# Kernel optimization log

Measured on AMD Instinct MI355X. Metric: run time of the kernel, lower is better.

## Reference

```python
import jax, jax.numpy as jnp
import numpy as np

B, S, HID, NH = 8, 1024, 1024, 16
HD = HID // NH


def setup_inputs() -> dict:
    key = jax.random.key(0)
    ks = jax.random.split(key, 7)
    scale = 1.0 / np.sqrt(HID)
    return {
        "x": jax.random.normal(ks[0], (B, S, HID), dtype=jnp.float32),
        "attention_mask": jax.random.uniform(ks[1], (B, 1, S, S), dtype=jnp.float32),
        "Wq": jax.random.normal(ks[2], (HID, HID), dtype=jnp.float32) * scale,
        "bq": jnp.zeros((HID,), jnp.float32),
        "Wk": jax.random.normal(ks[3], (HID, HID), dtype=jnp.float32) * scale,
        "bk": jnp.zeros((HID,), jnp.float32),
        "Wv": jax.random.normal(ks[4], (HID, HID), dtype=jnp.float32) * scale,
        "bv": jnp.zeros((HID,), jnp.float32),
        "Wp": jax.random.normal(ks[5], (HID, HID), dtype=jnp.float32) * scale,
        "bp": jnp.zeros((HID,), jnp.float32),
    }


def _split(t):
    # [B, S, HID] -> [B, NH, S, HD]
    b, s, _ = t.shape
    return t.reshape(b, s, NH, HD).transpose(0, 2, 1, 3)


def reference(x, attention_mask, Wq, bq, Wk, bk, Wv, bv, Wp, bp):
    q = _split(x @ Wq + bq)  # [B, NH, S, HD]
    k = _split(x @ Wk + bk)
    v = _split(x @ Wv + bv)
    # NOTE: module scales by rsqrt(full hidden_dim) = rsqrt(NH*HD), faithful to source
    scores = jnp.einsum("bhqd,bhkd->bhqk", q, k) * jax.lax.rsqrt(jnp.float32(HID))
    scores = scores + attention_mask * (-1e9)
    attn = jax.nn.softmax(scores, axis=-1)
    ctx = jnp.einsum("bhqk,bhkd->bhqd", attn, v)  # [B, NH, S, HD]
    ctx = ctx.transpose(0, 2, 1, 3).reshape(x.shape[0], x.shape[1], HID)
    # projection (Conv1D k=1 == dense); dropout is identity at inference
    return ctx @ Wp + bp
```

## Files before the change

kernel.cpp:

```cpp
#include <hip/hip_runtime.h>


using bf16x8 = __attribute__((ext_vector_type(8))) short;
using f32x4  = __attribute__((ext_vector_type(4))) float;

#define DEVFN __device__ __forceinline__

typedef const __attribute__((address_space(1))) void gas_void;
typedef __attribute__((address_space(3))) void las_void;

DEVFN void gload16(const void* g, void* l) {
  __builtin_amdgcn_global_load_lds((gas_void*)g, (las_void*)l, 16, 0, 0);
}

DEVFN unsigned short f2bf(float f) {
  union { float f; unsigned u; } v; v.f = f;
  unsigned r = v.u + 0x7fffu + ((v.u >> 16) & 1u);
  return (unsigned short)(r >> 16);
}

DEVFN unsigned cvtpk(float lo, float hi) {
  unsigned r;
  asm("v_cvt_pk_bf16_f32 %0, %1, %2" : "=v"(r) : "v"(lo), "v"(hi));
  return r;
}

__global__ __launch_bounds__(256) void k_convert_x(const float* __restrict__ x,
                                                   unsigned short* __restrict__ xb) {
  int i = (blockIdx.x * 256 + threadIdx.x) * 4;
  float4 v = *reinterpret_cast<const float4*>(x + i);
  ushort4 o;
  o.x = f2bf(v.x); o.y = f2bf(v.y); o.z = f2bf(v.z); o.w = f2bf(v.w);
  *reinterpret_cast<ushort4*>(xb + i) = o;
}

__global__ __launch_bounds__(256) void k_transpose_w(const float* __restrict__ Wq,
                                                     const float* __restrict__ Wk,
                                                     const float* __restrict__ Wv,
                                                     const float* __restrict__ Wp,
                                                     unsigned short* __restrict__ Wcat,
                                                     unsigned short* __restrict__ Wpt) {
  __shared__ float tile[64][65];
  int z = blockIdx.z;
  const float* W = (z == 0) ? Wq : (z == 1) ? Wk : (z == 2) ? Wv : Wp;
  unsigned short* out = (z == 3) ? Wpt : (Wcat + (size_t)z * 1024 * 1024);
  int k0 = blockIdx.y * 64, n0 = blockIdx.x * 64;
  int t = threadIdx.x;
  int tr = t >> 4, tc = (t & 15) * 4;
#pragma unroll
  for (int p = 0; p < 4; ++p) {
    int k = p * 16 + tr;
    float4 v = *reinterpret_cast<const float4*>(W + (size_t)(k0 + k) * 1024 + n0 + tc);
    tile[k][tc + 0] = v.x; tile[k][tc + 1] = v.y;
    tile[k][tc + 2] = v.z; tile[k][tc + 3] = v.w;
  }
  __syncthreads();
#pragma unroll
  for (int p = 0; p < 4; ++p) {
    int n = p * 16 + tr;
    ushort4 o;
    o.x = f2bf(tile[tc + 0][n]); o.y = f2bf(tile[tc + 1][n]);
    o.z = f2bf(tile[tc + 2][n]); o.w = f2bf(tile[tc + 3][n]);
    *reinterpret_cast<ushort4*>(out + (size_t)(n0 + n) * 1024 + k0 + tc) = o;
  }
}

template <int MODE>
__global__ __launch_bounds__(256) void k_gemm(const unsigned short* __restrict__ A,
                                              const unsigned short* __restrict__ Bt,
                                              const float* __restrict__ b0,
                                              const float* __restrict__ b1,
                                              const float* __restrict__ b2,
                                              unsigned short* __restrict__ Qb,
                                              unsigned short* __restrict__ Kb,
                                              unsigned short* __restrict__ Vtb,
                                              float* __restrict__ outp) {
  __shared__ unsigned short sm[128 * 128];
  unsigned short* As = sm;
  unsigned short* Bs = sm + 128 * 64;
  int t = threadIdx.x, lane = t & 63, w = t >> 6;
  int lgrp = lane >> 4, l16 = lane & 15;
  int n0 = blockIdx.x * 128, m0 = blockIdx.y * 128;
  int wm = w >> 1, wn = w & 1;
  const unsigned short* Ag = A + (size_t)m0 * 1024;
  const unsigned short* Bg = Bt + (size_t)n0 * 1024;

  const f32x4 zf = {0.f, 0.f, 0.f, 0.f};
  f32x4 acc[4][4];
#pragma unroll
  for (int mi = 0; mi < 4; ++mi)
#pragma unroll
    for (int ni = 0; ni < 4; ++ni) acc[mi][ni] = zf;

  for (int kt = 0; kt < 16; ++kt) {
    int kof = kt * 64;
#pragma unroll
    for (int is = 0; is < 4; ++is) {
      int ci = is * 256 + t;
      int row = ci >> 3, c = ci & 7;
      gload16(Ag + (size_t)row * 1024 + kof + c * 8, As + ci * 8);
      gload16(Bg + (size_t)row * 1024 + kof + c * 8, Bs + ci * 8);
    }
    __syncthreads();
    bf16x8 af[4][2], bfr[4][2];
#pragma unroll
    for (int mi = 0; mi < 4; ++mi)
#pragma unroll
      for (int s = 0; s < 2; ++s)
        af[mi][s] = *reinterpret_cast<const bf16x8*>(
            As + (wm * 64 + mi * 16 + l16) * 64 + s * 32 + lgrp * 8);
#pragma unroll
    for (int ni = 0; ni < 4; ++ni)
#pragma unroll
      for (int s = 0; s < 2; ++s)
        bfr[ni][s] = *reinterpret_cast<const bf16x8*>(
            Bs + (wn * 64 + ni * 16 + l16) * 64 + s * 32 + lgrp * 8);
#pragma unroll
    for (int mi = 0; mi < 4; ++mi)
#pragma unroll
      for (int ni = 0; ni < 4; ++ni)
#pragma unroll
        for (int s = 0; s < 2; ++s)
          acc[mi][ni] = __builtin_amdgcn_mfma_f32_16x16x32_bf16(
              af[mi][s], bfr[ni][s], acc[mi][ni], 0, 0, 0);
    __syncthreads();
  }

  if (MODE == 0) {
    int seg = n0 >> 10;
    int nn0 = n0 & 1023;
    const float* bias = (seg == 0) ? b0 : (seg == 1) ? b1 : b2;
    if (seg < 2) {
      unsigned short* o = (seg == 0) ? Qb : Kb;
#pragma unroll
      for (int ni = 0; ni < 4; ++ni) {
        int n = nn0 + wn * 64 + ni * 16 + l16;
        float bval = bias[n];
#pragma unroll
        for (int mi = 0; mi < 4; ++mi) {
          int ml = wm * 64 + mi * 16 + lgrp * 4;
#pragma unroll
          for (int r = 0; r < 4; ++r)
            o[(size_t)(m0 + ml + r) * 1024 + n] = f2bf(acc[mi][ni][r] + bval);
        }
      }
    } else {
#pragma unroll
      for (int ni = 0; ni < 4; ++ni) {
        int nl = wn * 64 + ni * 16 + l16;
        float bval = bias[nn0 + nl];
        int sw = (nl & 7) << 3;
#pragma unroll
        for (int mi = 0; mi < 4; ++mi) {
          int ml = wm * 64 + mi * 16 + lgrp * 4;
#pragma unroll
          for (int r = 0; r < 4; ++r)
            sm[nl * 128 + ((ml + r) ^ sw)] = f2bf(acc[mi][ni][r] + bval);
        }
      }
      __syncthreads();
      int bb = m0 >> 10, s0 = m0 & 1023;
      int nl = t >> 1, mh = (t & 1) * 64;
      int ng = nn0 + nl, hh = ng >> 6, d = ng & 63;
      unsigned short* vb = Vtb + ((size_t)(bb * 16 + hh) * 64 + d) * 1024 + s0;
      int sw = (nl & 7) << 3;
#pragma unroll
      for (int j = 0; j < 8; ++j) {
        int me = mh + j * 8;
        bf16x8 v = *reinterpret_cast<const bf16x8*>(sm + nl * 128 + (me ^ sw));
        *reinterpret_cast<bf16x8*>(vb + me) = v;
      }
    }
  } else {
#pragma unroll
    for (int ni = 0; ni < 4; ++ni) {
      int n = n0 + wn * 64 + ni * 16 + l16;
      float bval = b0[n];
#pragma unroll
      for (int mi = 0; mi < 4; ++mi) {
        int ml = wm * 64 + mi * 16 + lgrp * 4;
#pragma unroll
        for (int r = 0; r < 4; ++r)
          outp[(size_t)(m0 + ml + r) * 1024 + n] = acc[mi][ni][r] + bval;
      }
    }
  }
}

__global__ __launch_bounds__(256) void k_attn(const unsigned short* __restrict__ Qb,
                                              const unsigned short* __restrict__ Kb,
                                              const unsigned short* __restrict__ Vtb,
                                              const float* __restrict__ mask,
                                              unsigned short* __restrict__ ctx) {
  __shared__ unsigned short Qs[64 * 64];
  __shared__ unsigned short Ks[2][64 * 64];
  __shared__ unsigned short Vts[2][64 * 64];
  __shared__ unsigned short Ps[4][16 * 72];

  int t = threadIdx.x, lane = t & 63, w = t >> 6;
  int lgrp = lane >> 4, l16 = lane & 15;
  int gid = blockIdx.x;
  int xcd = gid & 7, ii = gid >> 3;
  int grp = (ii >> 4) * 8 + xcd;
  int h = ii & 15;
  int b = grp >> 4, qt = grp & 15;

  const unsigned short* Qg = Qb + ((size_t)(b * 1024 + qt * 64)) * 1024 + h * 64;
  const unsigned short* Kg = Kb + (size_t)b * 1024 * 1024 + h * 64;
  const unsigned short* Vg = Vtb + ((size_t)(b * 16 + h) * 64) * 1024;
  const float* mrow = mask + (size_t)b * 1024 * 1024 + (size_t)(qt * 64 + w * 16 + l16) * 1024;

#pragma unroll
  for (int is = 0; is < 2; ++is) {
    int ci = is * 256 + t, row = ci >> 3, c = ci & 7, cs = c ^ (row & 7);
    gload16(Qg + (size_t)row * 1024 + cs * 8, Qs + ci * 8);
    gload16(Kg + (size_t)row * 1024 + cs * 8, Ks[0] + ci * 8);
    gload16(Vg + (size_t)row * 1024 + cs * 8, Vts[0] + ci * 8);
  }
  float4 mkc[4], mkn[4];
#pragma unroll
  for (int ct = 0; ct < 4; ++ct)
    mkc[ct] = *reinterpret_cast<const float4*>(mrow + ct * 16 + lgrp * 4);
  __syncthreads();

  bf16x8 aq[2];
  {
    int row = w * 16 + l16;
#pragma unroll
    for (int s = 0; s < 2; ++s) {
      int c = (s * 4 + lgrp) ^ (row & 7);
      aq[s] = *reinterpret_cast<const bf16x8*>(Qs + row * 64 + c * 8);
    }
  }

  const f32x4 zf = {0.f, 0.f, 0.f, 0.f};
  f32x4 acc[4];
#pragma unroll
  for (int dt = 0; dt < 4; ++dt) acc[dt] = zf;
  float m_s = -__builtin_inff(), l_s = 0.f;
  int cur = 0;

  for (int kt = 0; kt < 16; ++kt) {
    if (kt < 15) {
#pragma unroll
      for (int is = 0; is < 2; ++is) {
        int ci = is * 256 + t, row = ci >> 3, c = ci & 7, cs = c ^ (row & 7);
        gload16(Kg + (size_t)(kt + 1) * 64 * 1024 + (size_t)row * 1024 + cs * 8,
                Ks[cur ^ 1] + ci * 8);
        gload16(Vg + (size_t)row * 1024 + (kt + 1) * 64 + cs * 8, Vts[cur ^ 1] + ci * 8);
      }
#pragma unroll
      for (int ct = 0; ct < 4; ++ct)
        mkn[ct] = *reinterpret_cast<const float4*>(mrow + (kt + 1) * 64 + ct * 16 + lgrp * 4);
    }

    float sc[16];
    float mx = -__builtin_inff();
#pragma unroll
    for (int ct = 0; ct < 4; ++ct) {
      f32x4 sac = zf;
#pragma unroll
      for (int s = 0; s < 2; ++s) {
        int row = ct * 16 + l16;
        int c = (s * 4 + lgrp) ^ (row & 7);
        bf16x8 ak = *reinterpret_cast<const bf16x8*>(Ks[cur] + row * 64 + c * 8);
        sac = __builtin_amdgcn_mfma_f32_16x16x32_bf16(ak, aq[s], sac, 0, 0, 0);
      }
      const float* mp = reinterpret_cast<const float*>(&mkc[ct]);
#pragma unroll
      for (int r = 0; r < 4; ++r) {
        float v = __fadd_rn(__fmul_rn(sac[r], 0.03125f), __fmul_rn(mp[r], -1e9f));
        sc[ct * 4 + r] = v;
        mx = fmaxf(mx, v);
      }
    }
    mx = fmaxf(mx, __shfl_xor(mx, 16, 64));
    mx = fmaxf(mx, __shfl_xor(mx, 32, 64));
    float mn = fmaxf(m_s, mx);
    float resc = __expf(m_s - mn);
    m_s = mn;
    float rs = 0.f;
#pragma unroll
    for (int i = 0; i < 16; ++i) {
      float p = __expf(sc[i] - mn);
      sc[i] = p;
      rs += p;
    }
    rs += __shfl_xor(rs, 16, 64);
    rs += __shfl_xor(rs, 32, 64);
    l_s = l_s * resc + rs;

    float racc[4];
#pragma unroll
    for (int r = 0; r < 4; ++r) racc[r] = __shfl(resc, lgrp * 4 + r, 64);
#pragma unroll
    for (int dt = 0; dt < 4; ++dt)
#pragma unroll
      for (int r = 0; r < 4; ++r) acc[dt][r] *= racc[r];

#pragma unroll
    for (int ct = 0; ct < 4; ++ct) {
      uint2 u;
      u.x = cvtpk(sc[ct * 4 + 0], sc[ct * 4 + 1]);
      u.y = cvtpk(sc[ct * 4 + 2], sc[ct * 4 + 3]);
      *reinterpret_cast<uint2*>(&Ps[w][l16 * 72 + ct * 16 + lgrp * 4]) = u;
    }
    asm volatile("" ::: "memory");

#pragma unroll
    for (int s = 0; s < 2; ++s) {
      bf16x8 ap = *reinterpret_cast<const bf16x8*>(&Ps[w][l16 * 72 + s * 32 + lgrp * 8]);
#pragma unroll
      for (int dt = 0; dt < 4; ++dt) {
        int row = dt * 16 + l16;
        int c = (s * 4 + lgrp) ^ (row & 7);
        bf16x8 bv_ = *reinterpret_cast<const bf16x8*>(Vts[cur] + row * 64 + c * 8);
        acc[dt] = __builtin_amdgcn_mfma_f32_16x16x32_bf16(ap, bv_, acc[dt], 0, 0, 0);
      }
    }
    __syncthreads();
    cur ^= 1;
#pragma unroll
    for (int ct = 0; ct < 4; ++ct) mkc[ct] = mkn[ct];
  }

  float linv[4];
#pragma unroll
  for (int r = 0; r < 4; ++r) linv[r] = 1.0f / __shfl(l_s, lgrp * 4 + r, 64);
  size_t mbase = (size_t)(b * 1024 + qt * 64 + w * 16 + lgrp * 4);
#pragma unroll
  for (int dt = 0; dt < 4; ++dt)
#pragma unroll
    for (int r = 0; r < 4; ++r)
      ctx[(mbase + r) * 1024 + h * 64 + dt * 16 + l16] = f2bf(acc[dt][r] * linv[r]);
}

extern "C" void kernel_launch(void* const* d_in, const int* in_sizes, int n_in,
                              void* d_out, int out_size, void* d_ws, size_t ws_size,
                              hipStream_t stream) {
  const float* x    = (const float*)d_in[0];
  const float* mask = (const float*)d_in[1];
  const float* Wq = (const float*)d_in[2];
  const float* bq = (const float*)d_in[3];
  const float* Wk = (const float*)d_in[4];
  const float* bk = (const float*)d_in[5];
  const float* Wv = (const float*)d_in[6];
  const float* bv = (const float*)d_in[7];
  const float* Wp = (const float*)d_in[8];
  const float* bp = (const float*)d_in[9];

  const size_t MB = 1u << 20;
  char* ws = (char*)d_ws;
  unsigned short* xbf  = (unsigned short*)(ws + 0);
  unsigned short* Wcat = (unsigned short*)(ws + 16 * MB);
  unsigned short* Wpt  = (unsigned short*)(ws + 22 * MB);
  unsigned short* Qb   = (unsigned short*)(ws + 24 * MB);
  unsigned short* Kb   = (unsigned short*)(ws + 40 * MB);
  unsigned short* Vtb  = (unsigned short*)(ws + 56 * MB);
  unsigned short* ctx  = xbf;

  k_convert_x<<<8192, 256, 0, stream>>>(x, xbf);
  k_transpose_w<<<dim3(16, 16, 4), 256, 0, stream>>>(Wq, Wk, Wv, Wp, Wcat, Wpt);
  k_gemm<0><<<dim3(24, 64), 256, 0, stream>>>(xbf, Wcat, bq, bk, bv, Qb, Kb, Vtb, nullptr);
  k_attn<<<2048, 256, 0, stream>>>(Qb, Kb, Vtb, mask, ctx);
  k_gemm<1><<<dim3(8, 64), 256, 0, stream>>>(ctx, Wpt, bp, nullptr, nullptr,
                                             nullptr, nullptr, nullptr, (float*)d_out);
}
```

Measured before the change: 342.0 us.

## Reuse Q LDS buffer for P, add setprio around MFMA, skip unneeded rescale

The attention kernel now stores the P tile in the Q shared buffer, with an XOR-swizzled layout, after Q is loaded into registers. This drops the separate padded P buffer and cuts LDS use, which may allow more resident blocks. s_setprio is raised around the two MFMA phases so matrix work gets scheduling priority over other waves. The online-softmax rescale of the accumulator is skipped when no row maximum grew anywhere in the wave, at the cost of an extra barrier and a wave-wide vote.

```diff
diff --git a/kernel.cpp b/kernel.cpp
--- a/kernel.cpp
+++ b/kernel.cpp
@@ -192,10 +192,9 @@
                                               const unsigned short* __restrict__ Vtb,
                                               const float* __restrict__ mask,
                                               unsigned short* __restrict__ ctx) {
-  __shared__ unsigned short Qs[64 * 64];
+  __shared__ unsigned short QPs[64 * 64];
   __shared__ unsigned short Ks[2][64 * 64];
   __shared__ unsigned short Vts[2][64 * 64];
-  __shared__ unsigned short Ps[4][16 * 72];
 
   int t = threadIdx.x, lane = t & 63, w = t >> 6;
   int lgrp = lane >> 4, l16 = lane & 15;
@@ -204,16 +203,17 @@
   int grp = (ii >> 4) * 8 + xcd;
   int h = ii & 15;
   int b = grp >> 4, qt = grp & 15;
+  int row64 = w * 16 + l16;
 
   const unsigned short* Qg = Qb + ((size_t)(b * 1024 + qt * 64)) * 1024 + h * 64;
   const unsigned short* Kg = Kb + (size_t)b * 1024 * 1024 + h * 64;
   const unsigned short* Vg = Vtb + ((size_t)(b * 16 + h) * 64) * 1024;
-  const float* mrow = mask + (size_t)b * 1024 * 1024 + (size_t)(qt * 64 + w * 16 + l16) * 1024;
+  const float* mrow = mask + (size_t)b * 1024 * 1024 + (size_t)(qt * 64 + row64) * 1024;
 
 #pragma unroll
   for (int is = 0; is < 2; ++is) {
     int ci = is * 256 + t, row = ci >> 3, c = ci & 7, cs = c ^ (row & 7);
-    gload16(Qg + (size_t)row * 1024 + cs * 8, Qs + ci * 8);
+    gload16(Qg + (size_t)row * 1024 + cs * 8, QPs + ci * 8);
     gload16(Kg + (size_t)row * 1024 + cs * 8, Ks[0] + ci * 8);
     gload16(Vg + (size_t)row * 1024 + cs * 8, Vts[0] + ci * 8);
   }
@@ -224,14 +224,12 @@
   __syncthreads();
 
   bf16x8 aq[2];
-  {
-    int row = w * 16 + l16;
-#pragma unroll
-    for (int s = 0; s < 2; ++s) {
-      int c = (s * 4 + lgrp) ^ (row & 7);
-      aq[s] = *reinterpret_cast<const bf16x8*>(Qs + row * 64 + c * 8);
-    }
-  }
+#pragma unroll
+  for (int s = 0; s < 2; ++s) {
+    int c = (s * 4 + lgrp) ^ (row64 & 7);
+    aq[s] = *reinterpret_cast<const bf16x8*>(QPs + row64 * 64 + c * 8);
+  }
+  __syncthreads();
 
   const f32x4 zf = {0.f, 0.f, 0.f, 0.f};
   f32x4 acc[4];
@@ -256,6 +254,7 @@
 
     float sc[16];
     float mx = -__builtin_inff();
+    __builtin_amdgcn_s_setprio(1);
 #pragma unroll
     for (int ct = 0; ct < 4; ++ct) {
       f32x4 sac = zf;
@@ -274,42 +273,55 @@
         mx = fmaxf(mx, v);
       }
     }
+    __builtin_amdgcn_s_setprio(0);
     mx = fmaxf(mx, __shfl_xor(mx, 16, 64));
     mx = fmaxf(mx, __shfl_xor(mx, 32, 64));
-    float mn = fmaxf(m_s, mx);
-    float resc = __expf(m_s - mn);
-    m_s = mn;
+
+    bool skip = __all(mx <= m_s) != 0;
+    float resc = 1.f;
+    if (!skip) {
+      float mn = fmaxf(m_s, mx);
+      resc = __expf(m_s - mn);
+      m_s = mn;
+    }
     float rs = 0.f;
 #pragma unroll
     for (int i = 0; i < 16; ++i) {
-      float p = __expf(sc[i] - mn);
+      float p = __expf(sc[i] - m_s);
       sc[i] = p;
       rs += p;
     }
     rs += __shfl_xor(rs, 16, 64);
     rs += __shfl_xor(rs, 32, 64);
-    l_s = l_s * resc + rs;
-
-    float racc[4];
-#pragma unroll
-    for (int r = 0; r < 4; ++r) racc[r] = __shfl(resc, lgrp * 4 + r, 64);
-#pragma unroll
-    for (int dt = 0; dt < 4; ++dt)
-#pragma unroll
-      for (int r = 0; r < 4; ++r) acc[dt][r] *= racc[r];
+    if (skip) {
+      l_s += rs;
+    } else {
+      l_s = l_s * resc + rs;
+      float racc[4];
+#pragma unroll
+      for (int r = 0; r < 4; ++r) racc[r] = __shfl(resc, lgrp * 4 + r, 64);
+#pragma unroll
+      for (int dt = 0; dt < 4; ++dt)
+#pragma unroll
+        for (int r = 0; r < 4; ++r) acc[dt][r] *= racc[r];
+    }
 
 #pragma unroll
     for (int ct = 0; ct < 4; ++ct) {
       uint2 u;
       u.x = cvtpk(sc[ct * 4 + 0], sc[ct * 4 + 1]);
       u.y = cvtpk(sc[ct * 4 + 2], sc[ct * 4 + 3]);
-      *reinterpret_cast<uint2*>(&Ps[w][l16 * 72 + ct * 16 + lgrp * 4]) = u;
+      int chunk = ct * 2 + (lgrp >> 1);
+      int ep = row64 * 64 + ((chunk ^ (l16 & 7)) << 3) + ((lgrp & 1) << 2);
+      *reinterpret_cast<uint2*>(&QPs[ep]) = u;
     }
     asm volatile("" ::: "memory");
 
+    __builtin_amdgcn_s_setprio(1);
 #pragma unroll
     for (int s = 0; s < 2; ++s) {
-      bf16x8 ap = *reinterpret_cast<const bf16x8*>(&Ps[w][l16 * 72 + s * 32 + lgrp * 8]);
+      int ec = row64 * 64 + (((s * 4 + lgrp) ^ (l16 & 7)) << 3);
+      bf16x8 ap = *reinterpret_cast<const bf16x8*>(&QPs[ec]);
 #pragma unroll
       for (int dt = 0; dt < 4; ++dt) {
         int row = dt * 16 + l16;
@@ -318,6 +330,7 @@
         acc[dt] = __builtin_amdgcn_mfma_f32_16x16x32_bf16(ap, bv_, acc[dt], 0, 0, 0);
       }
     }
+    __builtin_amdgcn_s_setprio(0);
     __syncthreads();
     cur ^= 1;
 #pragma unroll
```

New measurement: 328.6 us. 3.9% less time.
